# Kernel optimization log

Hardware: AMD Instinct MI355X
Metric: run time of the kernel (lower is better)

## Reference

```python
import jax, jax.numpy as jnp
import numpy as np

IN_F = 4096
OUT_F = 4096
BLOCK = 8
N_CENTROIDS = 2048
N_BLOCKS = IN_F // BLOCK  # 512
N_TOKENS = 1024


def setup_inputs() -> dict:
    key = jax.random.key(0)
    k1, k2, k3, k4 = jax.random.split(key, 4)
    x = jax.random.normal(k1, (N_TOKENS, IN_F), dtype=jnp.float32)
    centroids = jax.random.normal(k2, (N_CENTROIDS, BLOCK), dtype=jnp.float32)
    # assignments: block-major layout, length n_blocks * out_features
    assignments = jax.random.randint(k3, (N_BLOCKS * OUT_F,), 0, N_CENTROIDS, dtype=jnp.int32)
    bias = jax.random.normal(k4, (OUT_F,), dtype=jnp.float32) * 0.01
    # counts = bincount(assignments), used only in backward (grad averaging)
    counts = jax.ops.segment_sum(
        jnp.ones_like(assignments, dtype=jnp.float32), assignments,
        num_segments=N_CENTROIDS)
    return {"x": x, "centroids": centroids, "bias": bias,
            "assignments": assignments, "counts": counts}


def reference(x, centroids, bias, assignments, counts):
    # weight = centroids[assignments].reshape(n_blocks, out_f, block)
    #                        .permute(1,0,2).reshape(out_f, in_f)
    w = centroids[assignments]  # [n_blocks*out_f, block]
    w = w.reshape(N_BLOCKS, OUT_F, BLOCK).transpose(1, 0, 2).reshape(OUT_F, IN_F)
    # F.linear(x, weight, bias) = x @ w.T + bias
    return x @ w.T + bias
```

## Files before the change

### kernel.cpp

```cpp
#include <hip/hip_runtime.h>
#include <hip/hip_bf16.h>

#define IN_F   4096
#define OUT_F  4096
#define QBLK   8
#define NBLKS  512
#define NTOK   1024
#define NCENT  2048

#define SPLITK 4
#define KCHUNK (IN_F / SPLITK)
#define KITERS (KCHUNK / 32)

typedef unsigned int u32;
typedef unsigned short u16;
typedef __attribute__((ext_vector_type(8))) short short8;
typedef __attribute__((ext_vector_type(4))) float floatx4;

__device__ __forceinline__ u16 f2bf(float f) {
  union { float f; u32 u; } v; v.f = f;
  u32 u = v.u;
  return (u16)((u + 0x7fffu + ((u >> 16) & 1u)) >> 16);
}

__device__ __forceinline__ void load_lds_16(const void* g, void* l) {
  __builtin_amdgcn_global_load_lds(
      (const __attribute__((address_space(1))) u32*)g,
      (__attribute__((address_space(3))) u32*)l, 16, 0, 0);
}

__global__ __launch_bounds__(256) void cast_bf16_kernel(
    const float* __restrict__ src, u16* __restrict__ dst) {
  int g = blockIdx.x * 256 + threadIdx.x;
  const float4* sv = (const float4*)src;
  float4 a = sv[(size_t)g * 2];
  float4 b = sv[(size_t)g * 2 + 1];
  union { u16 s[8]; uint4 v; } o;
  o.s[0] = f2bf(a.x); o.s[1] = f2bf(a.y); o.s[2] = f2bf(a.z); o.s[3] = f2bf(a.w);
  o.s[4] = f2bf(b.x); o.s[5] = f2bf(b.y); o.s[6] = f2bf(b.z); o.s[7] = f2bf(b.w);
  ((uint4*)dst)[g] = o.v;
}

__global__ __launch_bounds__(256) void cast_swz_kernel(
    const float* __restrict__ src, u16* __restrict__ dst) {
  __shared__ __align__(16) u16 ls[256 * 8];
  const int b = blockIdx.x;
  const int mg = b >> 5;
  const int kq = b & 31;
  const int t = threadIdx.x;
  const int ml = t >> 4;
  const int kbl = t & 15;

  const float* p = src + (size_t)(mg * 16 + ml) * IN_F + kq * 128 + kbl * 8;
  float4 a = ((const float4*)p)[0];
  float4 c = ((const float4*)p)[1];
  union { u16 s[8]; uint4 v; } o;
  o.s[0] = f2bf(a.x); o.s[1] = f2bf(a.y); o.s[2] = f2bf(a.z); o.s[3] = f2bf(a.w);
  o.s[4] = f2bf(c.x); o.s[5] = f2bf(c.y); o.s[6] = f2bf(c.z); o.s[7] = f2bf(c.w);

  const int cidx = (kbl << 4) | (ml ^ kbl);
  *(uint4*)&ls[cidx * 8] = o.v;
  __syncthreads();

  const int g = (t & 0xF0) | ((t & 15) ^ ((t >> 4) & 15));
  uint4* dbase = (uint4*)(dst + (size_t)(mg * 512 + kq * 16) * 128);
  dbase[g] = ((const uint4*)ls)[t];
}

__global__ __launch_bounds__(256, 4) void gemm_fused_kernel(
    const u16* __restrict__ xs,
    const u16* __restrict__ centb,
    const int* __restrict__ assign,
    const float* __restrict__ bias,
    float* __restrict__ out0,
    float* __restrict__ partials) {
  __shared__ __align__(16) u16 cs[NCENT * 8];

  const int id = blockIdx.x;
  const int s = (id & 7) >> 1;
  const int tile = ((id >> 3) << 1) | (id & 1);
  const int n0 = (tile & 31) * 128;
  const int m0 = (tile >> 5) * 128;

  const int t = threadIdx.x;
  const int lane = t & 63;
  const int wv = t >> 6;
  const int wm = wv >> 1;
  const int wn = wv & 1;
  const int quad = lane >> 4;
  const int r16 = lane & 15;
  const int kb0 = (s * KCHUNK) >> 3;

#pragma unroll
  for (int it = 0; it < 8; ++it) {
    int c = it * 256 + t;
    load_lds_16(centb + (size_t)c * 8, cs + (size_t)c * 8);
  }

  floatx4 acc[4][4];
#pragma unroll
  for (int i = 0; i < 4; ++i)
#pragma unroll
    for (int j = 0; j < 4; ++j)
#pragma unroll
      for (int r = 0; r < 4; ++r) acc[i][j][r] = 0.0f;

  const int ncol = n0 + wn * 64 + r16;

  const char* xA = (const char*)xs +
      ((size_t)((m0 >> 4) + wm * 4) * 512 + kb0) * 256;
  const u32 va = (u32)(quad * 256 + r16 * 16);
  const int* ai = assign + (size_t)kb0 * OUT_F;
  const u32 vi = (u32)(quad * OUT_F + ncol);

  short8 afc[4];
  int idxc[4];
#pragma unroll
  for (int i = 0; i < 4; ++i)
    afc[i] = *(const short8*)(xA + (va + (u32)i * 131072u));
#pragma unroll
  for (int j = 0; j < 4; ++j) idxc[j] = ai[vi + (u32)(j * 16)];

  __syncthreads();

  const short8* csv = (const short8*)cs;
#pragma unroll 2
  for (int kt = 0; kt < KITERS; ++kt) {
    short8 afn[4];
    int idxn[4];
    if (kt + 1 < KITERS) {
      const char* xk = xA + (va + (u32)((kt + 1) * 1024));
#pragma unroll
      for (int i = 0; i < 4; ++i)
        afn[i] = *(const short8*)(xk + (u32)i * 131072u);
      const int* an = ai + (size_t)(kt + 1) * 4 * OUT_F;
#pragma unroll
      for (int j = 0; j < 4; ++j) idxn[j] = an[vi + (u32)(j * 16)];
    }

    short8 bfr[4];
#pragma unroll
    for (int j = 0; j < 4; ++j) bfr[j] = csv[idxc[j]];

#pragma unroll
    for (int i = 0; i < 4; ++i)
#pragma unroll
      for (int j = 0; j < 4; ++j)
        acc[i][j] = __builtin_amdgcn_mfma_f32_16x16x32_bf16(afc[i], bfr[j], acc[i][j], 0, 0, 0);

#pragma unroll
    for (int i = 0; i < 4; ++i) afc[i] = afn[i];
#pragma unroll
    for (int j = 0; j < 4; ++j) idxc[j] = idxn[j];
  }

  float* C = (s == 0) ? out0 : (partials + (size_t)(s - 1) * NTOK * OUT_F);
  const int row_base = m0 + wm * 64 + quad * 4;
#pragma unroll
  for (int j = 0; j < 4; ++j) {
    const int col = ncol + j * 16;
#pragma unroll
    for (int i = 0; i < 4; ++i) {
      const int row = row_base + i * 16;
#pragma unroll
      for (int r = 0; r < 4; ++r)
        C[(size_t)(row + r) * OUT_F + col] = acc[i][j][r];
    }
  }
}

__global__ __launch_bounds__(256) void reduce_kernel(
    float* __restrict__ out, const float* __restrict__ partials,
    const float* __restrict__ bias, int sm1) {
  int g = blockIdx.x * 256 + threadIdx.x;
  float4 v = ((const float4*)out)[g];
  for (int s = 0; s < sm1; ++s) {
    float4 p = ((const float4*)(partials + (size_t)s * NTOK * OUT_F))[g];
    v.x += p.x; v.y += p.y; v.z += p.z; v.w += p.w;
  }
  float4 b = ((const float4*)bias)[g & (OUT_F / 4 - 1)];
  v.x += b.x; v.y += b.y; v.z += b.z; v.w += b.w;
  ((float4*)out)[g] = v;
}

extern "C" void kernel_launch(void* const* d_in, const int* in_sizes, int n_in,
                              void* d_out, int out_size, void* d_ws, size_t ws_size,
                              hipStream_t stream) {
  const float* x      = (const float*)d_in[0];
  const float* cent   = (const float*)d_in[1];
  const float* bias   = (const float*)d_in[2];
  const int*   assign = (const int*)d_in[3];
  float* out = (float*)d_out;

  const size_t xb_bytes   = (size_t)NTOK * IN_F * sizeof(u16);
  const size_t cent_bytes = (size_t)NCENT * 8 * sizeof(u16);
  u16*   xs       = (u16*)d_ws;
  u16*   centb    = (u16*)((char*)d_ws + xb_bytes);
  float* partials = (float*)((char*)d_ws + xb_bytes + cent_bytes);

  hipLaunchKernelGGL(cast_swz_kernel, dim3(64 * 32), dim3(256), 0, stream, x, xs);
  hipLaunchKernelGGL(cast_bf16_kernel, dim3((NCENT * 8 / 8) / 256), dim3(256), 0, stream,
                     cent, centb);
  hipLaunchKernelGGL(gemm_fused_kernel, dim3(1024), dim3(256), 0, stream,
                     xs, centb, assign, bias, out, partials);
  hipLaunchKernelGGL(reduce_kernel, dim3((NTOK * OUT_F / 4) / 256), dim3(256), 0, stream,
                     out, partials, bias, SPLITK - 1);
}
```

Before: 127.4 us.

## Fuse centroid cast into GEMM and deepen software pipeline of index/A loads

Removes the separate centroid bf16 cast kernel; each GEMM block now loads the fp32 centroids and converts them into LDS itself, saving one launch and a round trip through the workspace. The main loop is restructured so that assignment indices are prefetched three iterations ahead and A fragments two ahead, with the LDS centroid gather for the next step issued right after the MFMAs. This hides global-load and LDS latency better, at the cost of more live registers and redundant centroid conversion work in every block.

```diff
diff --git a/kernel.cpp b/kernel.cpp
--- a/kernel.cpp
+++ b/kernel.cpp
@@ -21,24 +21,6 @@
   union { float f; u32 u; } v; v.f = f;
   u32 u = v.u;
   return (u16)((u + 0x7fffu + ((u >> 16) & 1u)) >> 16);
-}
-
-__device__ __forceinline__ void load_lds_16(const void* g, void* l) {
-  __builtin_amdgcn_global_load_lds(
-      (const __attribute__((address_space(1))) u32*)g,
-      (__attribute__((address_space(3))) u32*)l, 16, 0, 0);
-}
-
-__global__ __launch_bounds__(256) void cast_bf16_kernel(
-    const float* __restrict__ src, u16* __restrict__ dst) {
-  int g = blockIdx.x * 256 + threadIdx.x;
-  const float4* sv = (const float4*)src;
-  float4 a = sv[(size_t)g * 2];
-  float4 b = sv[(size_t)g * 2 + 1];
-  union { u16 s[8]; uint4 v; } o;
-  o.s[0] = f2bf(a.x); o.s[1] = f2bf(a.y); o.s[2] = f2bf(a.z); o.s[3] = f2bf(a.w);
-  o.s[4] = f2bf(b.x); o.s[5] = f2bf(b.y); o.s[6] = f2bf(b.z); o.s[7] = f2bf(b.w);
-  ((uint4*)dst)[g] = o.v;
 }
 
 __global__ __launch_bounds__(256) void cast_swz_kernel(
@@ -69,7 +51,7 @@
 
 __global__ __launch_bounds__(256, 4) void gemm_fused_kernel(
     const u16* __restrict__ xs,
-    const u16* __restrict__ centb,
+    const float* __restrict__ cent,
     const int* __restrict__ assign,
     const float* __restrict__ bias,
     float* __restrict__ out0,
@@ -91,10 +73,16 @@
   const int r16 = lane & 15;
   const int kb0 = (s * KCHUNK) >> 3;
 
+  const float4* cf = (const float4*)cent;
 #pragma unroll
   for (int it = 0; it < 8; ++it) {
     int c = it * 256 + t;
-    load_lds_16(centb + (size_t)c * 8, cs + (size_t)c * 8);
+    float4 a = cf[(size_t)c * 2];
+    float4 b = cf[(size_t)c * 2 + 1];
+    union { u16 h[8]; uint4 v; } o;
+    o.h[0] = f2bf(a.x); o.h[1] = f2bf(a.y); o.h[2] = f2bf(a.z); o.h[3] = f2bf(a.w);
+    o.h[4] = f2bf(b.x); o.h[5] = f2bf(b.y); o.h[6] = f2bf(b.z); o.h[7] = f2bf(b.w);
+    *(uint4*)&cs[(size_t)c * 8] = o.v;
   }
 
   floatx4 acc[4][4];
@@ -113,45 +101,54 @@
   const int* ai = assign + (size_t)kb0 * OUT_F;
   const u32 vi = (u32)(quad * OUT_F + ncol);
 
-  short8 afc[4];
-  int idxc[4];
+  int idx0[4], idxc[4], idxn[4];
+#pragma unroll
+  for (int j = 0; j < 4; ++j) idx0[j] = ai[vi + (u32)(j * 16)];
+  short8 afc[4], afn[4];
 #pragma unroll
   for (int i = 0; i < 4; ++i)
     afc[i] = *(const short8*)(xA + (va + (u32)i * 131072u));
 #pragma unroll
-  for (int j = 0; j < 4; ++j) idxc[j] = ai[vi + (u32)(j * 16)];
+  for (int i = 0; i < 4; ++i)
+    afn[i] = *(const short8*)(xA + (va + 1024u + (u32)i * 131072u));
+#pragma unroll
+  for (int j = 0; j < 4; ++j) idxc[j] = ai[(size_t)4 * OUT_F + vi + (u32)(j * 16)];
+#pragma unroll
+  for (int j = 0; j < 4; ++j) idxn[j] = ai[(size_t)8 * OUT_F + vi + (u32)(j * 16)];
 
   __syncthreads();
 
   const short8* csv = (const short8*)cs;
-#pragma unroll 2
+  short8 bfr[4];
+#pragma unroll
+  for (int j = 0; j < 4; ++j) bfr[j] = csv[idx0[j]];
+
   for (int kt = 0; kt < KITERS; ++kt) {
-    short8 afn[4];
-    int idxn[4];
+#pragma unroll
+    for (int j = 0; j < 4; ++j)
+#pragma unroll
+      for (int i = 0; i < 4; ++i)
+        acc[i][j] = __builtin_amdgcn_mfma_f32_16x16x32_bf16(afc[i], bfr[j], acc[i][j], 0, 0, 0);
+
     if (kt + 1 < KITERS) {
-      const char* xk = xA + (va + (u32)((kt + 1) * 1024));
+#pragma unroll
+      for (int j = 0; j < 4; ++j) bfr[j] = csv[idxc[j]];
+    }
+#pragma unroll
+    for (int j = 0; j < 4; ++j) idxc[j] = idxn[j];
+    if (kt + 3 < KITERS) {
+      const int* an = ai + (size_t)(kt + 3) * 4 * OUT_F;
+#pragma unroll
+      for (int j = 0; j < 4; ++j) idxn[j] = an[vi + (u32)(j * 16)];
+    }
+#pragma unroll
+    for (int i = 0; i < 4; ++i) afc[i] = afn[i];
+    if (kt + 2 < KITERS) {
+      const char* xk = xA + (va + (u32)((kt + 2) * 1024));
 #pragma unroll
       for (int i = 0; i < 4; ++i)
         afn[i] = *(const short8*)(xk + (u32)i * 131072u);
-      const int* an = ai + (size_t)(kt + 1) * 4 * OUT_F;
-#pragma unroll
-      for (int j = 0; j < 4; ++j) idxn[j] = an[vi + (u32)(j * 16)];
-    }
-
-    short8 bfr[4];
-#pragma unroll
-    for (int j = 0; j < 4; ++j) bfr[j] = csv[idxc[j]];
-
-#pragma unroll
-    for (int i = 0; i < 4; ++i)
-#pragma unroll
-      for (int j = 0; j < 4; ++j)
-        acc[i][j] = __builtin_amdgcn_mfma_f32_16x16x32_bf16(afc[i], bfr[j], acc[i][j], 0, 0, 0);
-
-#pragma unroll
-    for (int i = 0; i < 4; ++i) afc[i] = afn[i];
-#pragma unroll
-    for (int j = 0; j < 4; ++j) idxc[j] = idxn[j];
+    }
   }
 
   float* C = (s == 0) ? out0 : (partials + (size_t)(s - 1) * NTOK * OUT_F);
@@ -192,17 +189,13 @@
   const int*   assign = (const int*)d_in[3];
   float* out = (float*)d_out;
 
-  const size_t xb_bytes   = (size_t)NTOK * IN_F * sizeof(u16);
-  const size_t cent_bytes = (size_t)NCENT * 8 * sizeof(u16);
+  const size_t xb_bytes = (size_t)NTOK * IN_F * sizeof(u16);
   u16*   xs       = (u16*)d_ws;
-  u16*   centb    = (u16*)((char*)d_ws + xb_bytes);
-  float* partials = (float*)((char*)d_ws + xb_bytes + cent_bytes);
+  float* partials = (float*)((char*)d_ws + xb_bytes);
 
   hipLaunchKernelGGL(cast_swz_kernel, dim3(64 * 32), dim3(256), 0, stream, x, xs);
-  hipLaunchKernelGGL(cast_bf16_kernel, dim3((NCENT * 8 / 8) / 256), dim3(256), 0, stream,
-                     cent, centb);
   hipLaunchKernelGGL(gemm_fused_kernel, dim3(1024), dim3(256), 0, stream,
-                     xs, centb, assign, bias, out, partials);
+                     xs, cent, assign, bias, out, partials);
   hipLaunchKernelGGL(reduce_kernel, dim3((NTOK * OUT_F / 4) / 256), dim3(256), 0, stream,
                      out, partials, bias, SPLITK - 1);
 }
```

After: 150.6 us. +18.2%, slower.
